# Kernel optimization log

Hardware: AMD Instinct MI355X
Metric: run time of the kernel (lower is better)

## Reference

```python
import jax, jax.numpy as jnp
import numpy as np

D_MODEL = 1024
NUM_HEADS = 16
GROUP_SIZE = 4
NUM_GROUPS = NUM_HEADS // GROUP_SIZE  # 4
D_K = D_MODEL // NUM_HEADS            # 64
THETA = 10000.0
WINDOW = 512


def _rope(x, positions):
    # x: (..., t, d) with d even; interleaved-pair rotation, freq_i = theta^{-i/(d/2)}
    d = x.shape[-1]
    half = d // 2
    inv_freq = THETA ** (-jnp.arange(half, dtype=x.dtype) / half)          # (half,)
    ang = positions.astype(x.dtype)[:, None] * inv_freq[None, :]           # (t, half)
    cos, sin = jnp.cos(ang), jnp.sin(ang)
    x1, x2 = x[..., 0::2], x[..., 1::2]
    r1 = x1 * cos - x2 * sin
    r2 = x1 * sin + x2 * cos
    return jnp.stack([r1, r2], axis=-1).reshape(x.shape)


def setup_inputs() -> dict:
    key = jax.random.key(0)
    k1, k2, k3, k4, k5 = jax.random.split(key, 5)
    b, t = 2, 2048
    scale = 1.0 / np.sqrt(D_MODEL)
    return {
        "x": jax.random.normal(k1, (b, t, D_MODEL), dtype=jnp.float32),
        "WQ": jax.random.normal(k2, (D_MODEL, D_MODEL), dtype=jnp.float32) * scale,
        "WK": jax.random.normal(k3, (NUM_GROUPS * D_K, D_MODEL), dtype=jnp.float32) * scale,
        "WV": jax.random.normal(k4, (NUM_GROUPS * D_K, D_MODEL), dtype=jnp.float32) * scale,
        "WO": jax.random.normal(k5, (D_MODEL, D_MODEL), dtype=jnp.float32) * scale,
        "token_positions": jnp.arange(t, dtype=jnp.int32),
    }


def reference(x, WQ, WK, WV, WO, token_positions):
    b, t, _ = x.shape
    g, s, d = NUM_GROUPS, GROUP_SIZE, D_K
    # projections (Linear: y = x @ W^T, no bias)
    q = (x @ WQ.T).reshape(b, t, g, s, d).transpose(0, 2, 3, 1, 4)  # b g s t d
    k = (x @ WK.T).reshape(b, t, g, d).transpose(0, 2, 1, 3)        # b g t d
    v = (x @ WV.T).reshape(b, t, g, d).transpose(0, 2, 1, 3)        # b g t d
    q = _rope(q, token_positions)
    k = _rope(k, token_positions)
    # scores: kv heads shared across the s query heads of each group
    scores = jnp.einsum('bgsqd,bgkd->bgsqk', q, k) / jnp.sqrt(jnp.asarray(d, x.dtype))
    i = jnp.arange(t)[:, None]
    j = jnp.arange(t)[None, :]
    allowed = (i >= j) & (i - j <= WINDOW)  # causal sliding window
    scores = jnp.where(allowed, scores, -jnp.inf)
    probs = jax.nn.softmax(scores, axis=-1)
    out = jnp.einsum('bgsqk,bgkd->bgsqd', probs, v)                 # b g s t d
    out = out.transpose(0, 3, 1, 2, 4).reshape(b, t, D_MODEL)       # b t (g s d)
    return out @ WO.T
```

## Files before the change

### kernel.cpp

```cpp
#include <hip/hip_runtime.h>
#include <hip/hip_bf16.h>

typedef __bf16 bf16;
typedef __bf16 bf16x4 __attribute__((ext_vector_type(4)));
typedef __bf16 bf16x8 __attribute__((ext_vector_type(8)));
typedef float  floatx4 __attribute__((ext_vector_type(4)));

#define D_MODEL   1024
#define NUM_HEADS 16
#define NUM_GROUPS 4
#define DK        64
#define SEQ_T     2048
#define BATCH     2
#define M_ROWS    (BATCH*SEQ_T)
#define WINDOW    512
#define KV_DIM    (NUM_GROUPS*DK)
#define N_QKV     (D_MODEL + 2*KV_DIM)
#define QSCALE    0.1803368801111204f
#define FREQ_C    0.4152410118609203f

#define GLDS16(g, l)                                                          \
    __builtin_amdgcn_global_load_lds(                                         \
        (const __attribute__((address_space(1))) void*)(g),                   \
        (__attribute__((address_space(3))) void*)(l), 16, 0, 0)

__global__ __launch_bounds__(256)
void convert_all(const float* s0, bf16* d0, int c0,
                 const float* s1, bf16* d1, int c1,
                 const float* s2, bf16* d2, int c2,
                 const float* s3, bf16* d3, int c3,
                 const float* s4, bf16* d4, int c4)
{
    int id = blockIdx.x * 256 + threadIdx.x;
    const float* src; bf16* dst;
    if      (id < c0)         { src = s0; dst = d0; }
    else if ((id -= c0) < c1) { src = s1; dst = d1; }
    else if ((id -= c1) < c2) { src = s2; dst = d2; }
    else if ((id -= c2) < c3) { src = s3; dst = d3; }
    else if ((id -= c3) < c4) { src = s4; dst = d4; }
    else return;
    int i = id * 8;
    const float* s = src + i;
    float4 a = *(const float4*)s;
    float4 b = *(const float4*)(s + 4);
    bf16x8 v;
    v[0] = (bf16)a.x; v[1] = (bf16)a.y; v[2] = (bf16)a.z; v[3] = (bf16)a.w;
    v[4] = (bf16)b.x; v[5] = (bf16)b.y; v[6] = (bf16)b.z; v[7] = (bf16)b.w;
    *(bf16x8*)&dst[i] = v;
}

__global__ __launch_bounds__(256, 3)
void gemm_t64(const bf16* __restrict__ A, const bf16* __restrict__ W, int K,
              bf16* __restrict__ Cq, bf16* __restrict__ Ck, bf16* __restrict__ Vt,
              float* __restrict__ Co, const int* __restrict__ pos, int mode)
{
    __shared__ bf16 As[2][128 * 64];
    __shared__ bf16 Bs[2][64 * 64];

    const int tid  = threadIdx.x;
    const int wave = tid >> 6;
    const int lane = tid & 63;
    const int lr   = lane & 15;
    const int quad = lane >> 4;
    const int m0 = blockIdx.y * 128;
    const int n0 = blockIdx.x * 64;
    const int wm = (wave >> 1) * 64;
    const int wn = (wave & 1) * 32;

    const int cr8 = lane >> 3;
    const int cc  = ((lane & 7) ^ cr8) * 8;
    const bf16* Ag = &A[(size_t)(m0 + cr8) * K + cc];
    const bf16* Wg = &W[(size_t)(n0 + cr8) * K + cc];

#define STAGE(buf, kk)                                                        \
    do {                                                                      \
        GLDS16(Ag + (size_t)((wave * 4 + 0) * 8) * K + (kk), &As[buf][(wave * 4 + 0) * 512]); \
        GLDS16(Ag + (size_t)((wave * 4 + 1) * 8) * K + (kk), &As[buf][(wave * 4 + 1) * 512]); \
        GLDS16(Ag + (size_t)((wave * 4 + 2) * 8) * K + (kk), &As[buf][(wave * 4 + 2) * 512]); \
        GLDS16(Ag + (size_t)((wave * 4 + 3) * 8) * K + (kk), &As[buf][(wave * 4 + 3) * 512]); \
        GLDS16(Wg + (size_t)((wave * 2 + 0) * 8) * K + (kk), &Bs[buf][(wave * 2 + 0) * 512]); \
        GLDS16(Wg + (size_t)((wave * 2 + 1) * 8) * K + (kk), &Bs[buf][(wave * 2 + 1) * 512]); \
    } while (0)

    const int ax0 = (quad ^ (lane & 7)) * 8;
    const int ax1 = ax0 ^ 32;

    floatx4 acc[4][2];
#pragma unroll
    for (int i = 0; i < 4; i++)
#pragma unroll
        for (int j = 0; j < 2; j++) acc[i][j] = (floatx4)(0.0f);

    STAGE(0, 0);
    __asm__ volatile("s_waitcnt vmcnt(0)" ::: "memory");
    __builtin_amdgcn_s_barrier();

    int cur = 0;
    for (int k0 = 0; k0 < K; k0 += 64) {
        if (k0 + 64 < K) STAGE(cur ^ 1, k0 + 64);

        bf16x8 a0[4], a1[4], b0[2], b1[2];
#pragma unroll
        for (int mi = 0; mi < 4; mi++) {
            a0[mi] = *(const bf16x8*)&As[cur][(wm + mi * 16 + lr) * 64 + ax0];
            a1[mi] = *(const bf16x8*)&As[cur][(wm + mi * 16 + lr) * 64 + ax1];
        }
#pragma unroll
        for (int ni = 0; ni < 2; ni++) {
            b0[ni] = *(const bf16x8*)&Bs[cur][(wn + ni * 16 + lr) * 64 + ax0];
            b1[ni] = *(const bf16x8*)&Bs[cur][(wn + ni * 16 + lr) * 64 + ax1];
        }

#pragma unroll
        for (int mi = 0; mi < 4; mi++)
#pragma unroll
            for (int ni = 0; ni < 2; ni++) {
                acc[mi][ni] = __builtin_amdgcn_mfma_f32_16x16x32_bf16(
                    a0[mi], b0[ni], acc[mi][ni], 0, 0, 0);
                acc[mi][ni] = __builtin_amdgcn_mfma_f32_16x16x32_bf16(
                    a1[mi], b1[ni], acc[mi][ni], 0, 0, 0);
            }

        __asm__ volatile("s_waitcnt vmcnt(0)" ::: "memory");
        __builtin_amdgcn_s_barrier();
        cur ^= 1;
    }
#undef STAGE

    if (mode == 0) {
        if (n0 >= D_MODEL + KV_DIM) {
            const int g  = (n0 - (D_MODEL + KV_DIM)) >> 6;
            const int b  = m0 >> 11;
            const int bg = b * 4 + g;
#pragma unroll
            for (int mi = 0; mi < 4; mi++) {
#pragma unroll
                for (int ni = 0; ni < 2; ni++) {
                    int d  = wn + ni * 16 + lr;
                    int t0 = (m0 & (SEQ_T - 1)) + wm + mi * 16 + quad * 4;
                    bf16x4 v;
#pragma unroll
                    for (int r = 0; r < 4; r++) v[r] = (bf16)acc[mi][ni][r];
                    *(bf16x4*)&Vt[((size_t)(bg * 64 + d)) * SEQ_T + t0] = v;
                }
            }
        } else {
            bf16* out; int ld, coff; float sc;
            if (n0 < D_MODEL) { out = Cq; ld = D_MODEL; coff = n0; sc = QSCALE; }
            else              { out = Ck; ld = KV_DIM;  coff = n0 - D_MODEL; sc = 1.0f; }
            float inv[2];
            float sgn = (lr & 1) ? 1.0f : -1.0f;
#pragma unroll
            for (int ni = 0; ni < 2; ni++) {
                int ip = (wn + ni * 16 + lr) >> 1;
                inv[ni] = exp2f(-(float)ip * FREQ_C);
            }
#pragma unroll
            for (int mi = 0; mi < 4; mi++) {
#pragma unroll
                for (int r = 0; r < 4; r++) {
                    int row = m0 + wm + mi * 16 + quad * 4 + r;
                    float p = (float)pos[row & (SEQ_T - 1)];
#pragma unroll
                    for (int ni = 0; ni < 2; ni++) {
                        float v  = acc[mi][ni][r];
                        float vp = __shfl_xor(v, 1);
                        float ang = p * inv[ni];
                        float ss, cc2;
                        __sincosf(ang, &ss, &cc2);
                        v = v * cc2 + vp * ss * sgn;
                        out[(size_t)row * ld + coff + wn + ni * 16 + lr] = (bf16)(v * sc);
                    }
                }
            }
        }
    } else {
#pragma unroll
        for (int mi = 0; mi < 4; mi++)
#pragma unroll
            for (int ni = 0; ni < 2; ni++)
#pragma unroll
                for (int r = 0; r < 4; r++) {
                    int row = m0 + wm + mi * 16 + quad * 4 + r;
                    int col = n0 + wn + ni * 16 + lr;
                    Co[(size_t)row * D_MODEL + col] = acc[mi][ni][r];
                }
    }
}

__global__ __launch_bounds__(256)
void attn_mfma(const bf16* __restrict__ Q, const bf16* __restrict__ K,
               const bf16* __restrict__ Vt_g, bf16* __restrict__ AO)
{
    const int ST = 72;
    __shared__ bf16 Ks[64 * ST];
    __shared__ bf16 Vt[80 * ST];
    __shared__ bf16 Ps[4 * 32 * ST];

    const int tid  = threadIdx.x;
    const int wave = tid >> 6;
    const int lane = tid & 63;
    const int lr   = lane & 15;
    const int quad = lane >> 4;
    const int bg = blockIdx.y;
    const int b = bg >> 2, g = bg & 3;
    const int h = g * 4 + wave;
    const int q0 = blockIdx.x * 32;

    bf16x8 qf[2][2];
#pragma unroll
    for (int mi = 0; mi < 2; mi++)
#pragma unroll
        for (int ks = 0; ks < 2; ks++)
            qf[mi][ks] = *(const bf16x8*)
                &Q[((size_t)(b * SEQ_T + q0 + mi * 16 + lr)) * D_MODEL
                   + h * 64 + ks * 32 + quad * 8];

    for (int i = tid; i < 15 * ST; i += 256) Vt[65 * ST + i] = (bf16)0.0f;
    if (tid < ST) Vt[64 * ST + tid] = (bf16)(tid < 64 ? 1.0f : 0.0f);

    bf16* Pw = &Ps[wave * 32 * ST];

    floatx4 o[2][5];
#pragma unroll
    for (int mi = 0; mi < 2; mi++)
#pragma unroll
        for (int nt = 0; nt < 5; nt++) o[mi][nt] = (floatx4)(0.0f);

    const int t0   = (q0 >= WINDOW) ? ((q0 - WINDOW) & ~63) : 0;
    const int last = q0 & ~63;

    for (int j0 = t0; j0 <= last; j0 += 64) {
        const bool mC = (j0 == last);
        const bool mW = (q0 >= WINDOW) && (j0 == t0);
        __syncthreads();
#pragma unroll
        for (int i = 0; i < 2; i++) {
            int c = tid + i * 256;
            int row = c >> 3, col8 = (c & 7) * 8;
            *(bf16x8*)&Ks[row * ST + col8] =
                *(const bf16x8*)&K[((size_t)(b * SEQ_T + j0 + row)) * KV_DIM + g * 64 + col8];
            *(bf16x8*)&Vt[row * ST + col8] =
                *(const bf16x8*)&Vt_g[((size_t)(bg * 64 + row)) * SEQ_T + j0 + col8];
        }
        __syncthreads();

        floatx4 s[2][4];
#pragma unroll
        for (int mi = 0; mi < 2; mi++)
#pragma unroll
            for (int nt = 0; nt < 4; nt++) s[mi][nt] = (floatx4)(0.0f);
#pragma unroll
        for (int ks = 0; ks < 2; ks++) {
#pragma unroll
            for (int nt = 0; nt < 4; nt++) {
                bf16x8 kf = *(const bf16x8*)&Ks[(nt * 16 + lr) * ST + ks * 32 + quad * 8];
                s[0][nt] = __builtin_amdgcn_mfma_f32_16x16x32_bf16(qf[0][ks], kf, s[0][nt], 0, 0, 0);
                s[1][nt] = __builtin_amdgcn_mfma_f32_16x16x32_bf16(qf[1][ks], kf, s[1][nt], 0, 0, 0);
            }
        }

        if (mC) {
#pragma unroll
            for (int mi = 0; mi < 2; mi++)
#pragma unroll
                for (int nt = 0; nt < 4; nt++) {
                    int key = j0 + nt * 16 + lr;
#pragma unroll
                    for (int r = 0; r < 4; r++) {
                        int qi_ = q0 + mi * 16 + quad * 4 + r;
                        s[mi][nt][r] = (key <= qi_) ? s[mi][nt][r] : -1e30f;
                    }
                }
        } else if (mW) {
#pragma unroll
            for (int mi = 0; mi < 2; mi++)
#pragma unroll
                for (int nt = 0; nt < 4; nt++) {
                    int key = j0 + nt * 16 + lr;
#pragma unroll
                    for (int r = 0; r < 4; r++) {
                        int qi_ = q0 + mi * 16 + quad * 4 + r;
                        s[mi][nt][r] = (qi_ - key <= WINDOW) ? s[mi][nt][r] : -1e30f;
                    }
                }
        }

#pragma unroll
        for (int mi = 0; mi < 2; mi++)
#pragma unroll
            for (int nt = 0; nt < 4; nt++)
#pragma unroll
                for (int r = 0; r < 4; r++)
                    Pw[(mi * 16 + quad * 4 + r) * ST + nt * 16 + lr] =
                        (bf16)exp2f(s[mi][nt][r]);

        __asm__ volatile("s_waitcnt lgkmcnt(0)" ::: "memory");

#pragma unroll
        for (int ks = 0; ks < 2; ks++) {
            bf16x8 pf0 = *(const bf16x8*)&Pw[(0 + lr) * ST + ks * 32 + quad * 8];
            bf16x8 pf1 = *(const bf16x8*)&Pw[(16 + lr) * ST + ks * 32 + quad * 8];
#pragma unroll
            for (int nt = 0; nt < 5; nt++) {
                bf16x8 vf = *(const bf16x8*)&Vt[(nt * 16 + lr) * ST + ks * 32 + quad * 8];
                o[0][nt] = __builtin_amdgcn_mfma_f32_16x16x32_bf16(pf0, vf, o[0][nt], 0, 0, 0);
                o[1][nt] = __builtin_amdgcn_mfma_f32_16x16x32_bf16(pf1, vf, o[1][nt], 0, 0, 0);
            }
        }
    }

#pragma unroll
    for (int mi = 0; mi < 2; mi++)
#pragma unroll
        for (int r = 0; r < 4; r++) {
            float l = __shfl(o[mi][4][r], lane & 48);
            float invl = 1.0f / l;
            int row = q0 + mi * 16 + quad * 4 + r;
#pragma unroll
            for (int nt = 0; nt < 4; nt++)
                AO[((size_t)(b * SEQ_T + row)) * D_MODEL + h * 64 + nt * 16 + lr] =
                    (bf16)(o[mi][nt][r] * invl);
        }
}

extern "C" void kernel_launch(void* const* d_in, const int* in_sizes, int n_in,
                              void* d_out, int out_size, void* d_ws, size_t ws_size,
                              hipStream_t stream)
{
    const float* x  = (const float*)d_in[0];
    const float* WQ = (const float*)d_in[1];
    const float* WK = (const float*)d_in[2];
    const float* WV = (const float*)d_in[3];
    const float* WO = (const float*)d_in[4];
    const int*  pos = (const int*)d_in[5];

    char* ws   = (char*)d_ws;
    bf16* Qw   = (bf16*)ws;
    bf16* Kw   = (bf16*)(ws + (size_t) 8 * 1024 * 1024);
    bf16* Vt_g = (bf16*)(ws + (size_t)10 * 1024 * 1024);
    bf16* xb   = (bf16*)(ws + (size_t)12 * 1024 * 1024);
    bf16* AO   = xb;
    bf16* Wqkv = (bf16*)(ws + (size_t)20 * 1024 * 1024);
    bf16* WOb  = (bf16*)(ws + (size_t)23 * 1024 * 1024);

    const int cx = (M_ROWS * D_MODEL) / 8;
    const int cq = (D_MODEL * D_MODEL) / 8;
    const int ck = (KV_DIM * D_MODEL) / 8;
    const int ctot = cx + cq + 2 * ck + cq;
    convert_all<<<ctot / 256, 256, 0, stream>>>(
        x, xb, cx,
        WQ, Wqkv, cq,
        WK, Wqkv + (size_t)D_MODEL * D_MODEL, ck,
        WV, Wqkv + (size_t)(D_MODEL + KV_DIM) * D_MODEL, ck,
        WO, WOb, cq);

    gemm_t64<<<dim3(N_QKV / 64, M_ROWS / 128), 256, 0, stream>>>(
        xb, Wqkv, D_MODEL, Qw, Kw, Vt_g, nullptr, pos, 0);

    attn_mfma<<<dim3(SEQ_T / 32, BATCH * NUM_GROUPS), 256, 0, stream>>>(
        Qw, Kw, Vt_g, AO);

    gemm_t64<<<dim3(D_MODEL / 64, M_ROWS / 128), 256, 0, stream>>>(
        AO, WOb, D_MODEL, nullptr, nullptr, nullptr, (float*)d_out, pos, 1);
}
```

Baseline: 146.0 us.

## Keep attention probabilities in registers by transposing the score MFMA

Swaps the MFMA operands for the QK^T product so each lane holds scores in a layout usable directly as the A operand of the PV MFMA. This removes the per-wave LDS buffer for P, along with its write-then-read round trip and waitcnt. The V fragment loads are reshaped into two 4-element reads to match the permuted key ordering. It also adds a min-blocks hint of 3 to the launch bounds, which may constrain register allocation.

```diff
diff --git a/kernel.cpp b/kernel.cpp
--- a/kernel.cpp
+++ b/kernel.cpp
@@ -188,14 +188,13 @@
     }
 }
 
-__global__ __launch_bounds__(256)
+__global__ __launch_bounds__(256, 3)
 void attn_mfma(const bf16* __restrict__ Q, const bf16* __restrict__ K,
                const bf16* __restrict__ Vt_g, bf16* __restrict__ AO)
 {
     const int ST = 72;
     __shared__ bf16 Ks[64 * ST];
     __shared__ bf16 Vt[80 * ST];
-    __shared__ bf16 Ps[4 * 32 * ST];
 
     const int tid  = threadIdx.x;
     const int wave = tid >> 6;
@@ -219,8 +218,6 @@
     for (int i = tid; i < 15 * ST; i += 256) Vt[65 * ST + i] = (bf16)0.0f;
     if (tid < ST) Vt[64 * ST + tid] = (bf16)(tid < 64 ? 1.0f : 0.0f);
 
-    bf16* Pw = &Ps[wave * 32 * ST];
-
     floatx4 o[2][5];
 #pragma unroll
     for (int mi = 0; mi < 2; mi++)
@@ -245,67 +242,68 @@
         }
         __syncthreads();
 
-        floatx4 s[2][4];
-#pragma unroll
-        for (int mi = 0; mi < 2; mi++)
-#pragma unroll
-            for (int nt = 0; nt < 4; nt++) s[mi][nt] = (floatx4)(0.0f);
+        floatx4 s2[4][2];
+#pragma unroll
+        for (int nt = 0; nt < 4; nt++)
+#pragma unroll
+            for (int mi = 0; mi < 2; mi++) s2[nt][mi] = (floatx4)(0.0f);
 #pragma unroll
         for (int ks = 0; ks < 2; ks++) {
 #pragma unroll
             for (int nt = 0; nt < 4; nt++) {
                 bf16x8 kf = *(const bf16x8*)&Ks[(nt * 16 + lr) * ST + ks * 32 + quad * 8];
-                s[0][nt] = __builtin_amdgcn_mfma_f32_16x16x32_bf16(qf[0][ks], kf, s[0][nt], 0, 0, 0);
-                s[1][nt] = __builtin_amdgcn_mfma_f32_16x16x32_bf16(qf[1][ks], kf, s[1][nt], 0, 0, 0);
+                s2[nt][0] = __builtin_amdgcn_mfma_f32_16x16x32_bf16(kf, qf[0][ks], s2[nt][0], 0, 0, 0);
+                s2[nt][1] = __builtin_amdgcn_mfma_f32_16x16x32_bf16(kf, qf[1][ks], s2[nt][1], 0, 0, 0);
             }
         }
 
         if (mC) {
 #pragma unroll
-            for (int mi = 0; mi < 2; mi++)
-#pragma unroll
-                for (int nt = 0; nt < 4; nt++) {
-                    int key = j0 + nt * 16 + lr;
+            for (int nt = 0; nt < 4; nt++)
+#pragma unroll
+                for (int mi = 0; mi < 2; mi++) {
+                    int qi_ = q0 + mi * 16 + lr;
 #pragma unroll
                     for (int r = 0; r < 4; r++) {
-                        int qi_ = q0 + mi * 16 + quad * 4 + r;
-                        s[mi][nt][r] = (key <= qi_) ? s[mi][nt][r] : -1e30f;
+                        int key = j0 + nt * 16 + quad * 4 + r;
+                        s2[nt][mi][r] = (key <= qi_) ? s2[nt][mi][r] : -1e30f;
                     }
                 }
         } else if (mW) {
 #pragma unroll
-            for (int mi = 0; mi < 2; mi++)
-#pragma unroll
-                for (int nt = 0; nt < 4; nt++) {
-                    int key = j0 + nt * 16 + lr;
+            for (int nt = 0; nt < 4; nt++)
+#pragma unroll
+                for (int mi = 0; mi < 2; mi++) {
+                    int qi_ = q0 + mi * 16 + lr;
 #pragma unroll
                     for (int r = 0; r < 4; r++) {
-                        int qi_ = q0 + mi * 16 + quad * 4 + r;
-                        s[mi][nt][r] = (qi_ - key <= WINDOW) ? s[mi][nt][r] : -1e30f;
+                        int key = j0 + nt * 16 + quad * 4 + r;
+                        s2[nt][mi][r] = (qi_ - key <= WINDOW) ? s2[nt][mi][r] : -1e30f;
                     }
                 }
         }
 
+        bf16x8 pa[2][2];
 #pragma unroll
         for (int mi = 0; mi < 2; mi++)
 #pragma unroll
-            for (int nt = 0; nt < 4; nt++)
-#pragma unroll
-                for (int r = 0; r < 4; r++)
-                    Pw[(mi * 16 + quad * 4 + r) * ST + nt * 16 + lr] =
-                        (bf16)exp2f(s[mi][nt][r]);
-
-        __asm__ volatile("s_waitcnt lgkmcnt(0)" ::: "memory");
+            for (int ks = 0; ks < 2; ks++)
+#pragma unroll
+                for (int r = 0; r < 4; r++) {
+                    pa[mi][ks][r]     = (bf16)exp2f(s2[2 * ks][mi][r]);
+                    pa[mi][ks][r + 4] = (bf16)exp2f(s2[2 * ks + 1][mi][r]);
+                }
 
 #pragma unroll
         for (int ks = 0; ks < 2; ks++) {
-            bf16x8 pf0 = *(const bf16x8*)&Pw[(0 + lr) * ST + ks * 32 + quad * 8];
-            bf16x8 pf1 = *(const bf16x8*)&Pw[(16 + lr) * ST + ks * 32 + quad * 8];
 #pragma unroll
             for (int nt = 0; nt < 5; nt++) {
-                bf16x8 vf = *(const bf16x8*)&Vt[(nt * 16 + lr) * ST + ks * 32 + quad * 8];
-                o[0][nt] = __builtin_amdgcn_mfma_f32_16x16x32_bf16(pf0, vf, o[0][nt], 0, 0, 0);
-                o[1][nt] = __builtin_amdgcn_mfma_f32_16x16x32_bf16(pf1, vf, o[1][nt], 0, 0, 0);
+                const bf16* vb = &Vt[(nt * 16 + lr) * ST + ks * 32 + quad * 4];
+                bf16x4 vlo = *(const bf16x4*)vb;
+                bf16x4 vhi = *(const bf16x4*)(vb + 16);
+                bf16x8 vf = __builtin_shufflevector(vlo, vhi, 0, 1, 2, 3, 4, 5, 6, 7);
+                o[0][nt] = __builtin_amdgcn_mfma_f32_16x16x32_bf16(pa[0][ks], vf, o[0][nt], 0, 0, 0);
+                o[1][nt] = __builtin_amdgcn_mfma_f32_16x16x32_bf16(pa[1][ks], vf, o[1][nt], 0, 0, 0);
             }
         }
     }
```

Result: no change. 147.5 us (+1.0%).
